# Kernel tuning notes

Hardware: AMD Instinct MI355X
Metric: run time of the kernel (lower is better)

The kernel has to match this reference:

```python
import jax, jax.numpy as jnp
import numpy as np

B, S, D = 4, 2048, 1024
H, A = 16, 64  # num_heads, attention_depth
LN_EPS = 1e-3  # keras LayerNormalization default epsilon


def setup_inputs() -> dict:
    key = jax.random.key(0)
    ks = jax.random.split(key, 12)
    s_in = 1.0 / np.sqrt(D)
    return {
        "query_inputs": jax.random.normal(ks[0], (B, S, D), jnp.float32),
        "key_value_inputs": jax.random.normal(ks[1], (B, S, D), jnp.float32),
        "Wq": jax.random.normal(ks[2], (H, D, A), jnp.float32) * s_in,
        "bq": jnp.zeros((H, A), jnp.float32),
        "Wk": jax.random.normal(ks[3], (H, D, A), jnp.float32) * s_in,
        "bk": jnp.zeros((H, A), jnp.float32),
        "Wo": jax.random.normal(ks[4], (H, D, D), jnp.float32) * s_in,
        "bo": jnp.zeros((H, D), jnp.float32),
        "gamma": jnp.ones((D,), jnp.float32),
        "beta": jnp.zeros((D,), jnp.float32),
    }


def reference(query_inputs, key_value_inputs, Wq, bq, Wk, bk, Wo, bo, gamma, beta):
    sqrt_depth = jnp.sqrt(jnp.asarray(A, jnp.float32))
    # per-head Q/K projections, batched over heads: [B,H,S,A]
    q = (jnp.einsum("bsd,hda->bhsa", query_inputs, Wq) + bq[None, :, None, :]) / sqrt_depth
    k = jnp.einsum("btd,hda->bhta", key_value_inputs, Wk) + bk[None, :, None, :]
    # keras Attention: scores = q @ k^T (q already pre-scaled), causal mask
    scores = jnp.einsum("bhsa,bhta->bhst", q, k)
    causal = jnp.tril(jnp.ones((S, S), bool))
    scores = jnp.where(causal[None, None], scores, jnp.finfo(scores.dtype).min)
    weights = jax.nn.softmax(scores, axis=-1)
    # values are the raw key_value_inputs (model_dims channels)
    attn = jnp.einsum("bhst,btd->bhsd", weights, key_value_inputs)
    # per-head output dense with relu, then sum over heads (tf.add_n)
    head_out = jax.nn.relu(jnp.einsum("bhsd,hde->bhse", attn, Wo) + bo[None, :, None, :])
    attn_sum = head_out.sum(axis=1)  # [B,S,D]
    # dropout is identity in inference mode (training=False)
    x = query_inputs + attn_sum
    mean = x.mean(axis=-1, keepdims=True)
    var = x.var(axis=-1, keepdims=True)
    return gamma * (x - mean) * jax.lax.rsqrt(var + LN_EPS) + beta
```

## Files before the change

kernel.cpp:

```cpp
#include <hip/hip_runtime.h>
#include <stdint.h>

#define B_ 4
#define S_ 2048
#define D_ 1024
#define H_ 16
#define A_ 64
#define LN_EPS 1e-3f
#define L2E 1.4426950408889634f

typedef __bf16 bf16x8 __attribute__((ext_vector_type(8)));
typedef __bf16 bf16x4 __attribute__((ext_vector_type(4)));
typedef float f32x4 __attribute__((ext_vector_type(4)));

__device__ __forceinline__ f32x4 mfma16(bf16x8 a, bf16x8 b, f32x4 c) {
    return __builtin_amdgcn_mfma_f32_16x16x32_bf16(a, b, c, 0, 0, 0);
}
__device__ __forceinline__ void glds16(const void* g, void* l) {
    __builtin_amdgcn_global_load_lds(
        (const __attribute__((address_space(1))) void*)g,
        (__attribute__((address_space(3))) void*)l, 16, 0, 0);
}

#define SWZ(slot, r) ((slot) ^ (((r) & 1) << 2) ^ (((r) >> 1) & 3))
__device__ __forceinline__ void stage_half(const __bf16* __restrict__ src, size_t ld,
                                           __bf16* lhalf, int w, int lane) {
    #pragma unroll
    for (int i = 0; i < 2; ++i) {
        int ch = w * 2 + i;
        int r = ch * 8 + (lane >> 3);
        int sl = SWZ(lane & 7, r);
        glds16(src + (size_t)r * ld + sl * 8, lhalf + ch * 512);
    }
}
__device__ __forceinline__ bf16x8 fragS(const __bf16* h, int r, int ks, int fg) {
    return *(const bf16x8*)(h + r * 64 + SWZ(ks * 4 + fg, r) * 8);
}

__device__ __forceinline__ void glds_tile128(const __bf16* __restrict__ src, size_t ld,
                                             __bf16* lds, int w, int lane) {
    int r = lane >> 2;
    int c = (lane & 3) * 8;
    #pragma unroll
    for (int i = 0; i < 2; ++i) {
        int r0 = (w + i * 4) * 16;
        glds16(src + (size_t)(r0 + r) * ld + c, lds + r0 * 32);
    }
}
template <int NI, int NJ>
__device__ __forceinline__ void mfma_tileL(const __bf16* As, const __bf16* Bs,
                                           int wm, int wn, int fr, int fg,
                                           f32x4 (&acc)[NI][NJ]) {
    bf16x8 af[NI], bv[NJ];
    #pragma unroll
    for (int i = 0; i < NI; ++i)
        af[i] = *(const bf16x8*)(As + (wm + i * 16 + fr) * 32 + fg * 8);
    #pragma unroll
    for (int j = 0; j < NJ; ++j)
        bv[j] = *(const bf16x8*)(Bs + (wn + j * 16 + fr) * 32 + fg * 8);
    #pragma unroll
    for (int i = 0; i < NI; ++i)
        #pragma unroll
        for (int j = 0; j < NJ; ++j)
            acc[i][j] = mfma16(af[i], bv[j], acc[i][j]);
}

__global__ void k_tr_cvt(const float* __restrict__ in, __bf16* __restrict__ out,
                         int R, int C) {
    __shared__ float tile[32][33];
    size_t gbase = (size_t)blockIdx.z * R * C;
    int r0 = blockIdx.y * 32, c0 = blockIdx.x * 32;
    #pragma unroll
    for (int i = threadIdx.y; i < 32; i += 8)
        tile[i][threadIdx.x] = in[gbase + (size_t)(r0 + i) * C + c0 + threadIdx.x];
    __syncthreads();
    #pragma unroll
    for (int i = threadIdx.y; i < 32; i += 8)
        out[gbase + (size_t)(c0 + i) * R + r0 + threadIdx.x] = (__bf16)tile[threadIdx.x][i];
}
__global__ void k_tr_cvt2(const float* __restrict__ in0, const float* __restrict__ in1,
                          __bf16* __restrict__ out0, __bf16* __restrict__ out1,
                          int R, int C) {
    __shared__ float tile[32][33];
    int z = blockIdx.z;
    const float* in = (z < H_) ? in0 : in1;
    __bf16* out = (z < H_) ? out0 : out1;
    size_t gbase = (size_t)(z & (H_ - 1)) * R * C;
    int r0 = blockIdx.y * 32, c0 = blockIdx.x * 32;
    #pragma unroll
    for (int i = threadIdx.y; i < 32; i += 8)
        tile[i][threadIdx.x] = in[gbase + (size_t)(r0 + i) * C + c0 + threadIdx.x];
    __syncthreads();
    #pragma unroll
    for (int i = threadIdx.y; i < 32; i += 8)
        out[gbase + (size_t)(c0 + i) * R + r0 + threadIdx.x] = (__bf16)tile[threadIdx.x][i];
}

__global__ void k_cvt2(const float* __restrict__ in0, const float* __restrict__ in1,
                       __bf16* __restrict__ out0, __bf16* __restrict__ out1, int n8) {
    int i = blockIdx.x * blockDim.x + threadIdx.x;
    if (i >= n8) return;
    const float* in = blockIdx.y ? in1 : in0;
    __bf16* out = blockIdx.y ? out1 : out0;
    const float4* p = (const float4*)(in + (size_t)i * 8);
    float4 f0 = p[0], f1 = p[1];
    __bf16 v[8] = {(__bf16)f0.x, (__bf16)f0.y, (__bf16)f0.z, (__bf16)f0.w,
                   (__bf16)f1.x, (__bf16)f1.y, (__bf16)f1.z, (__bf16)f1.w};
    *(uint4*)(out + (size_t)i * 8) = *(const uint4*)v;
}

__global__ __launch_bounds__(256) void k_proj(
    const __bf16* __restrict__ qb, const __bf16* __restrict__ kvb,
    const __bf16* __restrict__ wqt, const __bf16* __restrict__ wkt,
    const float* __restrict__ bq, const float* __restrict__ bk,
    __bf16* __restrict__ qp, __bf16* __restrict__ kp) {
    __shared__ __bf16 As[2][128 * 32];
    __shared__ __bf16 Bs[2][128 * 32];
    int which = blockIdx.z;
    const __bf16* Ab = which ? kvb : qb;
    const __bf16* Bt = which ? wkt : wqt;
    const float* bias = which ? bk : bq;
    float scale = which ? 1.0f : 0.125f;
    __bf16* outp = which ? kp : qp;
    int m0 = blockIdx.y * 128, n0 = blockIdx.x * 128;
    int t = threadIdx.x, lane = t & 63, w = t >> 6;
    int wm = (w >> 1) * 64, wn = (w & 1) * 64;
    int fr = lane & 15, fg = lane >> 4;
    const __bf16* Abase = Ab + (size_t)m0 * D_;
    const __bf16* Bbase = Bt + (size_t)n0 * D_;
    f32x4 acc[4][4] = {};
    glds_tile128(Abase, D_, As[0], w, lane);
    glds_tile128(Bbase, D_, Bs[0], w, lane);
    __syncthreads();
    int cur = 0;
    const int nt = D_ / 32;
    for (int tt = 0; tt < nt; ++tt) {
        if (tt + 1 < nt) {
            glds_tile128(Abase + (tt + 1) * 32, D_, As[cur ^ 1], w, lane);
            glds_tile128(Bbase + (tt + 1) * 32, D_, Bs[cur ^ 1], w, lane);
        }
        mfma_tileL<4, 4>(As[cur], Bs[cur], wm, wn, fr, fg, acc);
        __syncthreads();
        cur ^= 1;
    }
    #pragma unroll
    for (int j = 0; j < 4; ++j) {
        int n = n0 + wn + j * 16 + fr;
        float bv = bias[n];
        #pragma unroll
        for (int i = 0; i < 4; ++i)
            #pragma unroll
            for (int jj = 0; jj < 4; ++jj) {
                int m = m0 + wm + i * 16 + fg * 4 + jj;
                outp[(size_t)m * (H_ * A_) + n] = (__bf16)((acc[i][j][jj] + bv) * scale);
            }
    }
}

__global__ __launch_bounds__(512, 1) void k_fattn(
    const __bf16* __restrict__ qpb, const __bf16* __restrict__ kpb,
    const __bf16* __restrict__ kvtb, __bf16* __restrict__ att) {
    __shared__ __bf16 Ks[64 * 64];
    __shared__ __bf16 Vs[2][4][128 * 64];
    __shared__ __bf16 Ps[128 * 64];
    __shared__ float lpar[128][2];
    int bid = blockIdx.x;
    int xcd = bid & 7, slot = bid >> 3;
    int n0 = (xcd & 1) * 512;
    int h = (xcd >> 1) * 4 + (slot >> 3);
    int yp = slot & 7;
    int t = threadIdx.x, lane = t & 63, w = t >> 6;
    int fr = lane & 15, fg = lane >> 4;
    int wr = w >> 2, wc = w & 3;
    int sr = w >> 1, sc = w & 1;
    const __bf16* Vb = kvtb + (size_t)n0 * S_;
    __bf16* ob = att + (size_t)h * S_ * D_;
    int kr = w * 8 + (lane >> 3);
    int ksl = SWZ(lane & 7, kr);

    #pragma unroll 1
    for (int seg = 0; seg < 2; ++seg) {
        int mt = seg ? (15 - yp) : yp;
        int m0 = mt * 128;
        int NT = (mt + 1) * 2;
        stage_half(qpb + (size_t)m0 * (H_ * A_) + h * A_, H_ * A_, Ps, w, lane);
        glds16(kpb + (size_t)kr * (H_ * A_) + h * A_ + ksl * 8, Ks + w * 512);
        asm volatile("s_waitcnt vmcnt(0)" ::: "memory");
        __builtin_amdgcn_s_barrier();
        bf16x8 qf[2][2];
        #pragma unroll
        for (int mi = 0; mi < 2; ++mi)
            #pragma unroll
            for (int ks = 0; ks < 2; ++ks)
                qf[mi][ks] = fragS(Ps, sr * 32 + mi * 16 + fr, ks, fg);
        asm volatile("s_waitcnt lgkmcnt(0)" ::: "memory");
        #pragma unroll
        for (int q = 0; q < 4; ++q)
            stage_half(Vb + (size_t)(q * 128) * S_, S_, &Vs[0][q][0], w, lane);
        uint4 kreg = {0, 0, 0, 0};
        if (NT > 1)
            kreg = *(const uint4*)(kpb + (size_t)(64 + kr) * (H_ * A_) + h * A_ + ksl * 8);
        __builtin_amdgcn_s_barrier();
        __builtin_amdgcn_sched_barrier(0);
        f32x4 acc[4][8] = {};
        float lsum[2][4] = {};
        int cur = 0;
        for (int tt = 0; tt < NT; ++tt) {
            bool pre = (tt + 1 < NT);
            if (pre) {
                asm volatile("s_waitcnt vmcnt(1)" ::: "memory");
            } else {
                asm volatile("s_waitcnt vmcnt(0)" ::: "memory");
            }
            asm volatile("s_waitcnt lgkmcnt(0)" ::: "memory");
            __builtin_amdgcn_s_barrier();
            __builtin_amdgcn_sched_barrier(0);
            if (pre) {
                #pragma unroll
                for (int q = 0; q < 4; ++q)
                    stage_half(Vb + (size_t)(q * 128) * S_ + (tt + 1) * 64, S_,
                               &Vs[cur ^ 1][q][0], w, lane);
            }
            f32x4 sac[2][2] = {};
            __builtin_amdgcn_s_setprio(1);
            #pragma unroll
            for (int ks = 0; ks < 2; ++ks)
                #pragma unroll
                for (int nj = 0; nj < 2; ++nj) {
                    bf16x8 kf = fragS(Ks, sc * 32 + nj * 16 + fr, ks, fg);
                    #pragma unroll
                    for (int mi = 0; mi < 2; ++mi)
                        sac[mi][nj] = mfma16(qf[mi][ks], kf, sac[mi][nj]);
                }
            __builtin_amdgcn_s_setprio(0);
            bool dg = (tt >= 2 * mt);
            if (dg) {
                #pragma unroll
                for (int mi = 0; mi < 2; ++mi)
                    #pragma unroll
                    for (int nj = 0; nj < 2; ++nj)
                        #pragma unroll
                        for (int jj = 0; jj < 4; ++jj) {
                            int srow = sr * 32 + mi * 16 + fg * 4 + jj;
                            int col = sc * 32 + nj * 16 + fr;
                            float p = exp2f(sac[mi][nj][jj] * L2E);
                            if (tt * 64 + col > m0 + srow) p = 0.f;
                            lsum[mi][jj] += p;
                            Ps[srow * 64 + (col ^ (fg << 4))] = (__bf16)p;
                        }
            } else {
                #pragma unroll
                for (int mi = 0; mi < 2; ++mi)
                    #pragma unroll
                    for (int nj = 0; nj < 2; ++nj)
                        #pragma unroll
                        for (int jj = 0; jj < 4; ++jj) {
                            int srow = sr * 32 + mi * 16 + fg * 4 + jj;
                            int col = sc * 32 + nj * 16 + fr;
                            float p = exp2f(sac[mi][nj][jj] * L2E);
                            lsum[mi][jj] += p;
                            Ps[srow * 64 + (col ^ (fg << 4))] = (__bf16)p;
                        }
            }
            asm volatile("s_waitcnt lgkmcnt(0)" ::: "memory");
            __builtin_amdgcn_s_barrier();
            __builtin_amdgcn_sched_barrier(0);
            if (pre) {
                asm volatile("s_waitcnt vmcnt(8)" ::: "memory");
                *(uint4*)(Ks + w * 512 + lane * 8) = kreg;
                if (tt + 2 < NT)
                    kreg = *(const uint4*)(kpb + (size_t)((tt + 2) * 64 + kr) * (H_ * A_) +
                                           h * A_ + ksl * 8);
            }
            __builtin_amdgcn_s_setprio(1);
            const __bf16* Vh = &Vs[cur][wc][0];
            #pragma unroll
            for (int ks = 0; ks < 2; ++ks) {
                bf16x8 pa[4], vf[8];
                #pragma unroll
                for (int mi = 0; mi < 4; ++mi) {
                    int r = wr * 64 + mi * 16 + fr;
                    int g = (ks * 4 + fg) ^ (((fr >> 2) & 3) << 1);
                    pa[mi] = *(const bf16x8*)(Ps + r * 64 + g * 8);
                }
                #pragma unroll
                for (int nj = 0; nj < 8; ++nj)
                    vf[nj] = fragS(Vh, nj * 16 + fr, ks, fg);
                #pragma unroll
                for (int mi = 0; mi < 4; ++mi)
                    #pragma unroll
                    for (int nj = 0; nj < 8; ++nj)
                        acc[mi][nj] = mfma16(pa[mi], vf[nj], acc[mi][nj]);
            }
            __builtin_amdgcn_s_setprio(0);
            __builtin_amdgcn_sched_barrier(0);
            cur ^= 1;
        }
        #pragma unroll
        for (int mi = 0; mi < 2; ++mi)
            #pragma unroll
            for (int jj = 0; jj < 4; ++jj) {
                float v = lsum[mi][jj];
                v += __shfl_xor(v, 1);
                v += __shfl_xor(v, 2);
                v += __shfl_xor(v, 4);
                v += __shfl_xor(v, 8);
                if (fr == 0) lpar[sr * 32 + mi * 16 + fg * 4 + jj][sc] = v;
            }
        asm volatile("s_waitcnt lgkmcnt(0)" ::: "memory");
        __builtin_amdgcn_s_barrier();
        #pragma unroll
        for (int mi = 0; mi < 4; ++mi)
            #pragma unroll
            for (int jj = 0; jj < 4; ++jj) {
                int row = wr * 64 + mi * 16 + fg * 4 + jj;
                float il = 1.f / (lpar[row][0] + lpar[row][1]);
                int m = m0 + row;
                #pragma unroll
                for (int nj = 0; nj < 8; ++nj) {
                    int n = n0 + wc * 128 + nj * 16 + fr;
                    ob[(size_t)m * D_ + n] = (__bf16)(acc[mi][nj][jj] * il);
                }
            }
        __builtin_amdgcn_s_barrier();
    }
}

__global__ __launch_bounds__(512) void k_headsum(
    const __bf16* __restrict__ att, const __bf16* __restrict__ Wot,
    const float* __restrict__ bo, __bf16* __restrict__ asum) {
    __shared__ __bf16 L[2][4][8192];
    int bid = blockIdx.x;
    int xcd = bid & 7, slot = bid >> 3;
    int p = xcd * 2 + (slot >> 5);
    int rem = slot & 31;
    int mt = rem >> 2;
    int n0 = (rem & 3) * 256;
    int m0 = mt * 256;
    int t = threadIdx.x, lane = t & 63, w = t >> 6;
    int wr = w >> 2, wc = w & 3;
    int fr = lane & 15, fg = lane >> 4;
    const __bf16* Ab = att + ((size_t)p * S_ + m0) * D_;
    const __bf16* Bb = Wot + ((size_t)p * D_ + n0) * D_;
    float bv4[4];
    #pragma unroll
    for (int j = 0; j < 4; ++j)
        bv4[j] = bo[(size_t)p * D_ + n0 + wc * 64 + j * 16 + fr];
    f32x4 acc[8][4] = {};
    auto stg = [&](int tt, int h, int buf) {
        const __bf16* s = (h < 2) ? (Ab + (size_t)(h * 128) * D_ + tt * 64)
                                  : (Bb + (size_t)((h - 2) * 128) * D_ + tt * 64);
        stage_half(s, D_, &L[buf][h][0], w, lane);
    };
    auto loads = [&](const __bf16* Ah, const __bf16* Bh, int rb0, int mh, int nh,
                     bf16x8 (&af)[4][2], bf16x8 (&bv)[2][2]) {
        #pragma unroll
        for (int i = 0; i < 4; ++i)
            #pragma unroll
            for (int ks = 0; ks < 2; ++ks)
                af[i][ks] = fragS(Ah, mh * 64 + i * 16 + fr, ks, fg);
        #pragma unroll
        for (int j = 0; j < 2; ++j)
            #pragma unroll
            for (int ks = 0; ks < 2; ++ks)
                bv[j][ks] = fragS(Bh, rb0 + nh * 32 + j * 16 + fr, ks, fg);
    };
    stg(0, 0, 0); stg(0, 1, 0); stg(0, 2, 0); stg(0, 3, 0);
    int cur = 0;
    const int nt = D_ / 64;
    for (int tt = 0; tt < nt; ++tt) {
        bool pre = (tt + 1 < nt);
        const __bf16* Ah = &L[cur][wr][0];
        const __bf16* Bh = &L[cur][2 + (wc >> 1)][0];
        int rb0 = (wc & 1) * 64;
        #pragma unroll
        for (int ph = 0; ph < 4; ++ph) {
            const int mh = ph >> 1, nh = ph & 1;
            bf16x8 af[4][2], bv[2][2];
            if (ph == 0) {
                if (pre) {
                    stg(tt + 1, 0, cur ^ 1);
                    stg(tt + 1, 1, cur ^ 1);
                    stg(tt + 1, 2, cur ^ 1);
                    stg(tt + 1, 3, cur ^ 1);
                    asm volatile("s_waitcnt vmcnt(8)" ::: "memory");
                } else {
                    asm volatile("s_waitcnt vmcnt(0)" ::: "memory");
                }
                __builtin_amdgcn_s_barrier();
                __builtin_amdgcn_sched_barrier(0);
                loads(Ah, Bh, rb0, mh, nh, af, bv);
            } else {
                loads(Ah, Bh, rb0, mh, nh, af, bv);
                __builtin_amdgcn_s_barrier();
                __builtin_amdgcn_sched_barrier(0);
            }
            __builtin_amdgcn_s_setprio(1);
            #pragma unroll
            for (int i = 0; i < 4; ++i)
                #pragma unroll
                for (int j = 0; j < 2; ++j) {
                    acc[mh * 4 + i][nh * 2 + j] =
                        mfma16(af[i][0], bv[j][0], acc[mh * 4 + i][nh * 2 + j]);
                    acc[mh * 4 + i][nh * 2 + j] =
                        mfma16(af[i][1], bv[j][1], acc[mh * 4 + i][nh * 2 + j]);
                }
            __builtin_amdgcn_s_setprio(0);
            __builtin_amdgcn_sched_barrier(0);
            __builtin_amdgcn_s_barrier();
        }
        cur ^= 1;
    }
    __bf16* dst = asum + ((size_t)p * S_ + m0) * D_;
    #pragma unroll
    for (int mi = 0; mi < 8; ++mi)
        #pragma unroll
        for (int jj = 0; jj < 4; ++jj) {
            int mr = wr * 128 + mi * 16 + fg * 4 + jj;
            #pragma unroll
            for (int nj = 0; nj < 4; ++nj) {
                int nc = n0 + wc * 64 + nj * 16 + fr;
                dst[(size_t)mr * D_ + nc] = (__bf16)fmaxf(acc[mi][nj][jj] + bv4[nj], 0.f);
            }
        }
}

__global__ __launch_bounds__(256) void k_ln(
    const float* __restrict__ x1b, const __bf16* __restrict__ parts,
    const float* __restrict__ gamma, const float* __restrict__ beta,
    float* __restrict__ outb) {
    int row = blockIdx.x;
    size_t base = (size_t)row * D_;
    int c = threadIdx.x * 4;
    float4 a = *(const float4*)(x1b + base + c);
    float x[4] = {a.x, a.y, a.z, a.w};
    #pragma unroll
    for (int p = 0; p < H_; ++p) {
        bf16x4 v = *(const bf16x4*)(parts + ((size_t)p * S_ + row) * D_ + c);
        x[0] += (float)v[0]; x[1] += (float)v[1];
        x[2] += (float)v[2]; x[3] += (float)v[3];
    }
    float sm = x[0] + x[1] + x[2] + x[3];
    float s2 = x[0] * x[0] + x[1] * x[1] + x[2] * x[2] + x[3] * x[3];
    #pragma unroll
    for (int m = 32; m >= 1; m >>= 1) {
        sm += __shfl_xor(sm, m);
        s2 += __shfl_xor(s2, m);
    }
    __shared__ float r1[4], r2[4];
    int w = threadIdx.x >> 6;
    if ((threadIdx.x & 63) == 0) { r1[w] = sm; r2[w] = s2; }
    __syncthreads();
    sm = r1[0] + r1[1] + r1[2] + r1[3];
    s2 = r2[0] + r2[1] + r2[2] + r2[3];
    float mean = sm * (1.f / D_);
    float var = s2 * (1.f / D_) - mean * mean;
    float rstd = rsqrtf(var + LN_EPS);
    #pragma unroll
    for (int jj = 0; jj < 4; ++jj)
        outb[base + c + jj] = gamma[c + jj] * (x[jj] - mean) * rstd + beta[c + jj];
}

extern "C" void kernel_launch(void* const* d_in, const int* in_sizes, int n_in,
                              void* d_out, int out_size, void* d_ws, size_t ws_size,
                              hipStream_t stream) {
    (void)in_sizes; (void)n_in; (void)out_size; (void)ws_size;
    const float* qin   = (const float*)d_in[0];
    const float* kvin  = (const float*)d_in[1];
    const float* Wq    = (const float*)d_in[2];
    const float* bq    = (const float*)d_in[3];
    const float* Wk    = (const float*)d_in[4];
    const float* bk    = (const float*)d_in[5];
    const float* Wo    = (const float*)d_in[6];
    const float* bo    = (const float*)d_in[7];
    const float* gamma = (const float*)d_in[8];
    const float* beta  = (const float*)d_in[9];
    float* out = (float*)d_out;
    char* ws = (char*)d_ws;

    size_t off = 0;
    auto alloc = [&](size_t bytes) {
        size_t o = off;
        off += (bytes + 255) & ~(size_t)255;
        return o;
    };
    size_t o_wqt = alloc((size_t)H_ * A_ * D_ * 2);
    size_t o_wkt = alloc((size_t)H_ * A_ * D_ * 2);
    size_t o_wot = alloc((size_t)H_ * D_ * D_ * 2);
    size_t o_kvt = alloc((size_t)B_ * D_ * S_ * 2);
    size_t o_qp  = alloc((size_t)B_ * S_ * H_ * A_ * 2);
    size_t o_kp  = alloc((size_t)B_ * S_ * H_ * A_ * 2);
    size_t o_att = alloc((size_t)H_ * S_ * D_ * 2);
    size_t xbytes_qb = (size_t)B_ * S_ * D_ * 2 * 2;
    size_t xbytes_as = (size_t)H_ * S_ * D_ * 2;
    size_t o_x = alloc(xbytes_qb > xbytes_as ? xbytes_qb : xbytes_as);

    __bf16* wqt = (__bf16*)(ws + o_wqt);
    __bf16* wkt = (__bf16*)(ws + o_wkt);
    __bf16* wot = (__bf16*)(ws + o_wot);
    __bf16* kvt = (__bf16*)(ws + o_kvt);
    __bf16* qp  = (__bf16*)(ws + o_qp);
    __bf16* kp  = (__bf16*)(ws + o_kp);
    __bf16* att = (__bf16*)(ws + o_att);
    __bf16* qb  = (__bf16*)(ws + o_x);
    __bf16* kvb = qb + (size_t)B_ * S_ * D_;
    __bf16* asum = (__bf16*)(ws + o_x);

    k_tr_cvt2<<<dim3(A_ / 32, D_ / 32, 2 * H_), dim3(32, 8), 0, stream>>>(
        Wq, Wk, wqt, wkt, D_, A_);
    k_tr_cvt<<<dim3(D_ / 32, D_ / 32, H_), dim3(32, 8), 0, stream>>>(Wo, wot, D_, D_);
    k_tr_cvt<<<dim3(D_ / 32, S_ / 32, B_), dim3(32, 8), 0, stream>>>(kvin, kvt, S_, D_);
    int n8 = B_ * S_ * D_ / 8;
    k_cvt2<<<dim3((n8 + 255) / 256, 2), 256, 0, stream>>>(qin, kvin, qb, kvb, n8);
    k_proj<<<dim3(8, 64, 2), 256, 0, stream>>>(qb, kvb, wqt, wkt, bq, bk, qp, kp);

    for (int b = 0; b < B_; ++b) {
        const __bf16* qpb  = qp + (size_t)b * S_ * (H_ * A_);
        const __bf16* kpb  = kp + (size_t)b * S_ * (H_ * A_);
        const __bf16* kvtb = kvt + (size_t)b * D_ * S_;
        k_fattn<<<256, 512, 0, stream>>>(qpb, kpb, kvtb, att);
        k_headsum<<<512, 512, 0, stream>>>(att, wot, bo, asum);
        k_ln<<<S_, 256, 0, stream>>>(qin + (size_t)b * S_ * D_, asum, gamma, beta,
                                     out + (size_t)b * S_ * D_);
    }
}
```

Before: 1.044 ms.

## Fuse fp32-to-bf16 input conversion into projection GEMM and double-buffer K tiles

Removes the separate k_cvt2 conversion kernel: k_proj now loads fp32 query/kv tiles into registers, converts them to bf16 and writes them to LDS, so the bf16 copies are never written to or read back from global memory. The 1/sqrt(A) scale is multiplied by log2(e), which removes a multiply per element in the attention softmax exp2. The K tile in flash attention switches from a register-staged prefetch to a double-buffered LDS buffer filled with global_load_lds, and lpar now aliases the P buffer. The trade-off is fp32 loads going through registers in the GEMM, which adds register pressure, and a wait for all outstanding loads (vmcnt(0)) on every attention iteration.

```diff
diff --git a/kernel.cpp b/kernel.cpp
--- a/kernel.cpp
+++ b/kernel.cpp
@@ -7,7 +7,6 @@
 #define H_ 16
 #define A_ 64
 #define LN_EPS 1e-3f
-#define L2E 1.4426950408889634f
 
 typedef __bf16 bf16x8 __attribute__((ext_vector_type(8)));
 typedef __bf16 bf16x4 __attribute__((ext_vector_type(4)));
@@ -96,50 +95,59 @@
         out[gbase + (size_t)(c0 + i) * R + r0 + threadIdx.x] = (__bf16)tile[threadIdx.x][i];
 }
 
-__global__ void k_cvt2(const float* __restrict__ in0, const float* __restrict__ in1,
-                       __bf16* __restrict__ out0, __bf16* __restrict__ out1, int n8) {
-    int i = blockIdx.x * blockDim.x + threadIdx.x;
-    if (i >= n8) return;
-    const float* in = blockIdx.y ? in1 : in0;
-    __bf16* out = blockIdx.y ? out1 : out0;
-    const float4* p = (const float4*)(in + (size_t)i * 8);
-    float4 f0 = p[0], f1 = p[1];
-    __bf16 v[8] = {(__bf16)f0.x, (__bf16)f0.y, (__bf16)f0.z, (__bf16)f0.w,
-                   (__bf16)f1.x, (__bf16)f1.y, (__bf16)f1.z, (__bf16)f1.w};
-    *(uint4*)(out + (size_t)i * 8) = *(const uint4*)v;
-}
-
 __global__ __launch_bounds__(256) void k_proj(
-    const __bf16* __restrict__ qb, const __bf16* __restrict__ kvb,
+    const float* __restrict__ qin, const float* __restrict__ kvin,
     const __bf16* __restrict__ wqt, const __bf16* __restrict__ wkt,
     const float* __restrict__ bq, const float* __restrict__ bk,
     __bf16* __restrict__ qp, __bf16* __restrict__ kp) {
     __shared__ __bf16 As[2][128 * 32];
     __shared__ __bf16 Bs[2][128 * 32];
     int which = blockIdx.z;
-    const __bf16* Ab = which ? kvb : qb;
+    const float* Af = which ? kvin : qin;
     const __bf16* Bt = which ? wkt : wqt;
     const float* bias = which ? bk : bq;
-    float scale = which ? 1.0f : 0.125f;
+    float scale = which ? 1.0f : 0.18033688011112042f;
     __bf16* outp = which ? kp : qp;
     int m0 = blockIdx.y * 128, n0 = blockIdx.x * 128;
     int t = threadIdx.x, lane = t & 63, w = t >> 6;
     int wm = (w >> 1) * 64, wn = (w & 1) * 64;
     int fr = lane & 15, fg = lane >> 4;
-    const __bf16* Abase = Ab + (size_t)m0 * D_;
+    const float* Abase = Af + (size_t)m0 * D_;
     const __bf16* Bbase = Bt + (size_t)n0 * D_;
+    uint4 areg[2];
+    auto loadA = [&](int k0) {
+        #pragma unroll
+        for (int i = 0; i < 2; ++i) {
+            int id = t + i * 256, row = id >> 2, ch = (id & 3) * 8;
+            const float* p = Abase + (size_t)row * D_ + k0 + ch;
+            float4 f0 = *(const float4*)p;
+            float4 f1 = *(const float4*)(p + 4);
+            __bf16 v8[8] = {(__bf16)f0.x, (__bf16)f0.y, (__bf16)f0.z, (__bf16)f0.w,
+                            (__bf16)f1.x, (__bf16)f1.y, (__bf16)f1.z, (__bf16)f1.w};
+            areg[i] = *(const uint4*)v8;
+        }
+    };
+    auto writeA = [&](__bf16* dst) {
+        #pragma unroll
+        for (int i = 0; i < 2; ++i) {
+            int id = t + i * 256, row = id >> 2, ch = (id & 3) * 8;
+            *(uint4*)(dst + row * 32 + ch) = areg[i];
+        }
+    };
     f32x4 acc[4][4] = {};
-    glds_tile128(Abase, D_, As[0], w, lane);
+    loadA(0);
     glds_tile128(Bbase, D_, Bs[0], w, lane);
+    writeA(As[0]);
     __syncthreads();
     int cur = 0;
     const int nt = D_ / 32;
     for (int tt = 0; tt < nt; ++tt) {
         if (tt + 1 < nt) {
-            glds_tile128(Abase + (tt + 1) * 32, D_, As[cur ^ 1], w, lane);
+            loadA((tt + 1) * 32);
             glds_tile128(Bbase + (tt + 1) * 32, D_, Bs[cur ^ 1], w, lane);
         }
         mfma_tileL<4, 4>(As[cur], Bs[cur], wm, wn, fr, fg, acc);
+        if (tt + 1 < nt) writeA(As[cur ^ 1]);
         __syncthreads();
         cur ^= 1;
     }
@@ -160,10 +168,10 @@
 __global__ __launch_bounds__(512, 1) void k_fattn(
     const __bf16* __restrict__ qpb, const __bf16* __restrict__ kpb,
     const __bf16* __restrict__ kvtb, __bf16* __restrict__ att) {
-    __shared__ __bf16 Ks[64 * 64];
+    __shared__ __bf16 Ks[2][64 * 64];
     __shared__ __bf16 Vs[2][4][128 * 64];
     __shared__ __bf16 Ps[128 * 64];
-    __shared__ float lpar[128][2];
+    float (*lpar)[2] = (float(*)[2])Ps;
     int bid = blockIdx.x;
     int xcd = bid & 7, slot = bid >> 3;
     int n0 = (xcd & 1) * 512;
@@ -184,7 +192,7 @@
         int m0 = mt * 128;
         int NT = (mt + 1) * 2;
         stage_half(qpb + (size_t)m0 * (H_ * A_) + h * A_, H_ * A_, Ps, w, lane);
-        glds16(kpb + (size_t)kr * (H_ * A_) + h * A_ + ksl * 8, Ks + w * 512);
+        glds16(kpb + (size_t)kr * (H_ * A_) + h * A_ + ksl * 8, &Ks[0][w * 512]);
         asm volatile("s_waitcnt vmcnt(0)" ::: "memory");
         __builtin_amdgcn_s_barrier();
         bf16x8 qf[2][2];
@@ -197,9 +205,6 @@
         #pragma unroll
         for (int q = 0; q < 4; ++q)
             stage_half(Vb + (size_t)(q * 128) * S_, S_, &Vs[0][q][0], w, lane);
-        uint4 kreg = {0, 0, 0, 0};
-        if (NT > 1)
-            kreg = *(const uint4*)(kpb + (size_t)(64 + kr) * (H_ * A_) + h * A_ + ksl * 8);
         __builtin_amdgcn_s_barrier();
         __builtin_amdgcn_sched_barrier(0);
         f32x4 acc[4][8] = {};
@@ -207,11 +212,7 @@
         int cur = 0;
         for (int tt = 0; tt < NT; ++tt) {
             bool pre = (tt + 1 < NT);
-            if (pre) {
-                asm volatile("s_waitcnt vmcnt(1)" ::: "memory");
-            } else {
-                asm volatile("s_waitcnt vmcnt(0)" ::: "memory");
-            }
+            asm volatile("s_waitcnt vmcnt(0)" ::: "memory");
             asm volatile("s_waitcnt lgkmcnt(0)" ::: "memory");
             __builtin_amdgcn_s_barrier();
             __builtin_amdgcn_sched_barrier(0);
@@ -220,6 +221,8 @@
                 for (int q = 0; q < 4; ++q)
                     stage_half(Vb + (size_t)(q * 128) * S_ + (tt + 1) * 64, S_,
                                &Vs[cur ^ 1][q][0], w, lane);
+                glds16(kpb + (size_t)((tt + 1) * 64 + kr) * (H_ * A_) + h * A_ + ksl * 8,
+                       &Ks[(tt + 1) & 1][w * 512]);
             }
             f32x4 sac[2][2] = {};
             __builtin_amdgcn_s_setprio(1);
@@ -227,7 +230,7 @@
             for (int ks = 0; ks < 2; ++ks)
                 #pragma unroll
                 for (int nj = 0; nj < 2; ++nj) {
-                    bf16x8 kf = fragS(Ks, sc * 32 + nj * 16 + fr, ks, fg);
+                    bf16x8 kf = fragS(&Ks[tt & 1][0], sc * 32 + nj * 16 + fr, ks, fg);
                     #pragma unroll
                     for (int mi = 0; mi < 2; ++mi)
                         sac[mi][nj] = mfma16(qf[mi][ks], kf, sac[mi][nj]);
@@ -243,7 +246,7 @@
                         for (int jj = 0; jj < 4; ++jj) {
                             int srow = sr * 32 + mi * 16 + fg * 4 + jj;
                             int col = sc * 32 + nj * 16 + fr;
-                            float p = exp2f(sac[mi][nj][jj] * L2E);
+                            float p = exp2f(sac[mi][nj][jj]);
                             if (tt * 64 + col > m0 + srow) p = 0.f;
                             lsum[mi][jj] += p;
                             Ps[srow * 64 + (col ^ (fg << 4))] = (__bf16)p;
@@ -257,7 +260,7 @@
                         for (int jj = 0; jj < 4; ++jj) {
                             int srow = sr * 32 + mi * 16 + fg * 4 + jj;
                             int col = sc * 32 + nj * 16 + fr;
-                            float p = exp2f(sac[mi][nj][jj] * L2E);
+                            float p = exp2f(sac[mi][nj][jj]);
                             lsum[mi][jj] += p;
                             Ps[srow * 64 + (col ^ (fg << 4))] = (__bf16)p;
                         }
@@ -265,13 +268,6 @@
             asm volatile("s_waitcnt lgkmcnt(0)" ::: "memory");
             __builtin_amdgcn_s_barrier();
             __builtin_amdgcn_sched_barrier(0);
-            if (pre) {
-                asm volatile("s_waitcnt vmcnt(8)" ::: "memory");
-                *(uint4*)(Ks + w * 512 + lane * 8) = kreg;
-                if (tt + 2 < NT)
-                    kreg = *(const uint4*)(kpb + (size_t)((tt + 2) * 64 + kr) * (H_ * A_) +
-                                           h * A_ + ksl * 8);
-            }
             __builtin_amdgcn_s_setprio(1);
             const __bf16* Vh = &Vs[cur][wc][0];
             #pragma unroll
@@ -296,6 +292,8 @@
             __builtin_amdgcn_sched_barrier(0);
             cur ^= 1;
         }
+        asm volatile("s_waitcnt lgkmcnt(0)" ::: "memory");
+        __builtin_amdgcn_s_barrier();
         #pragma unroll
         for (int mi = 0; mi < 2; ++mi)
             #pragma unroll
@@ -491,9 +489,7 @@
     size_t o_qp  = alloc((size_t)B_ * S_ * H_ * A_ * 2);
     size_t o_kp  = alloc((size_t)B_ * S_ * H_ * A_ * 2);
     size_t o_att = alloc((size_t)H_ * S_ * D_ * 2);
-    size_t xbytes_qb = (size_t)B_ * S_ * D_ * 2 * 2;
-    size_t xbytes_as = (size_t)H_ * S_ * D_ * 2;
-    size_t o_x = alloc(xbytes_qb > xbytes_as ? xbytes_qb : xbytes_as);
+    size_t o_as  = alloc((size_t)H_ * S_ * D_ * 2);
 
     __bf16* wqt = (__bf16*)(ws + o_wqt);
     __bf16* wkt = (__bf16*)(ws + o_wkt);
@@ -502,17 +498,13 @@
     __bf16* qp  = (__bf16*)(ws + o_qp);
     __bf16* kp  = (__bf16*)(ws + o_kp);
     __bf16* att = (__bf16*)(ws + o_att);
-    __bf16* qb  = (__bf16*)(ws + o_x);
-    __bf16* kvb = qb + (size_t)B_ * S_ * D_;
-    __bf16* asum = (__bf16*)(ws + o_x);
+    __bf16* asum = (__bf16*)(ws + o_as);
 
     k_tr_cvt2<<<dim3(A_ / 32, D_ / 32, 2 * H_), dim3(32, 8), 0, stream>>>(
         Wq, Wk, wqt, wkt, D_, A_);
     k_tr_cvt<<<dim3(D_ / 32, D_ / 32, H_), dim3(32, 8), 0, stream>>>(Wo, wot, D_, D_);
     k_tr_cvt<<<dim3(D_ / 32, S_ / 32, B_), dim3(32, 8), 0, stream>>>(kvin, kvt, S_, D_);
-    int n8 = B_ * S_ * D_ / 8;
-    k_cvt2<<<dim3((n8 + 255) / 256, 2), 256, 0, stream>>>(qin, kvin, qb, kvb, n8);
-    k_proj<<<dim3(8, 64, 2), 256, 0, stream>>>(qb, kvb, wqt, wkt, bq, bk, qp, kp);
+    k_proj<<<dim3(8, 64, 2), 256, 0, stream>>>(qin, kvin, wqt, wkt, bq, bk, qp, kp);
 
     for (int b = 0; b < B_; ++b) {
         const __bf16* qpb  = qp + (size_t)b * S_ * (H_ * A_);
```

Result: no change. 1.062 ms (+1.7%).
